# Optimization experiments

Measured on AMD Instinct MI355X. Metric: run time of the kernel, lower is better.

The kernel has to match this reference:

```python
import jax, jax.numpy as jnp
import numpy as np

N_QUBITS = 12
LAYERS = 3


def _apply(state, mats, axes):
    """Apply batched k-qubit gate. state: [B]+[2]*n complex64; mats: [B, 2^k, 2^k]; axes: state axes (1-based)."""
    k = len(axes)
    d = 2 ** k
    s = jnp.moveaxis(state, axes, tuple(range(1, k + 1)))
    shp = s.shape
    s = jnp.einsum('bij,bjk->bik', mats, s.reshape(shp[0], d, -1))
    return jnp.moveaxis(s.reshape(shp), tuple(range(1, k + 1)), axes)


def _ry(theta):
    # RY(theta) = [[cos(t/2), -sin(t/2)], [sin(t/2), cos(t/2)]], batched over B
    c = jnp.cos(theta / 2).astype(jnp.complex64)
    s = jnp.sin(theta / 2).astype(jnp.complex64)
    return jnp.stack([jnp.stack([c, -s], -1), jnp.stack([s, c], -1)], -2)


def _crx(theta):
    # CRX: identity on control=0 subspace, RX(theta) on control=1 subspace (basis order |ct>)
    c = jnp.cos(theta / 2).astype(jnp.complex64)
    s = (-1j) * jnp.sin(theta / 2).astype(jnp.complex64)
    o = jnp.ones_like(c)
    z = jnp.zeros_like(c)
    rows = [[o, z, z, z], [z, o, z, z], [z, z, c, s], [z, z, s, c]]
    return jnp.stack([jnp.stack(r, -1) for r in rows], -2)


def _circuit(state_re, state_im, params):
    B = params.shape[0]
    n = N_QUBITS
    state = (state_re + 1j * state_im).astype(jnp.complex64).reshape((B,) + (2,) * n)
    p = params.reshape(B, LAYERS, 4, n)  # param idx order: RY block, CRX block, RY block, CRX block
    for l in range(LAYERS):
        th = p[:, l]
        for w in range(n):
            state = _apply(state, _ry(th[:, 0, w]), (w + 1,))
        for i, w in enumerate(reversed(range(n))):
            state = _apply(state, _crx(th[:, 1, i]), (w + 1, ((w + 1) % n) + 1))
        for w in range(n):
            state = _apply(state, _ry(th[:, 2, w]), (w + 1,))
        for i, w in enumerate([n - 1] + list(range(n - 1))):
            state = _apply(state, _crx(th[:, 3, i]), (w + 1, ((w - 1) % n) + 1))
    state = state.reshape(B, -1)
    return jnp.stack([state.real, state.imag], -1)  # [B, 2^n, 2]


def setup_inputs() -> dict:
    key = jax.random.key(0)
    k1, k2, k3 = jax.random.split(key, 3)
    B = 128
    dim = 2 ** N_QUBITS
    return {
        'state_re': jax.random.normal(k1, (B, dim), jnp.float32),
        'state_im': jax.random.normal(k2, (B, dim), jnp.float32),
        'params': jax.random.normal(k3, (B, LAYERS * 4 * N_QUBITS), jnp.float32),
    }


def reference(state_re, state_im, params):
    return _circuit(state_re, state_im, params)
```

## Files before the change

### kernel.cpp

```cpp
#include <hip/hip_runtime.h>
#include <math.h>

#define DIM  4096
#define BLK  512
#define NPAR 144

typedef float v2f __attribute__((ext_vector_type(2)));

struct Ph { int reg[3]; int wav[3]; };
struct TMap { unsigned pk[9]; unsigned short so[8]; unsigned short rn[8]; };

constexpr int REGS[12][3] = {
  {11,0,1},{1,2,3},{3,4,5},{5,6,7},{7,8,9},{9,10,11},
  {11,0,1},{9,10,11},{7,8,9},{5,6,7},{3,4,5},{1,2,3}};

constexpr Ph phaseAt(int i) {
  Ph p = {};
  if (i == 0 || i == 37) {
    p.reg[0]=0; p.reg[1]=1; p.reg[2]=2;
    p.wav[0]=9; p.wav[1]=10; p.wav[2]=11;
    return p;
  }
  int e = (i - 1) % 12;
  for (int j = 0; j < 3; ++j) p.reg[j] = REGS[e][j];
  bool A = (e <= 2) || (e >= 10);
  p.wav[0] = A ? 6 : 2; p.wav[1] = A ? 7 : 3; p.wav[2] = A ? 8 : 4;
  return p;
}
constexpr bool inArr(const int* a, int n, int b) {
  for (int i = 0; i < n; ++i) if (a[i] == b) return true;
  return false;
}
constexpr bool isLoc(int t) {
  if (t == 0 || t == 36) return false;
  Ph a = phaseAt(t), b = phaseAt(t + 1);
  return a.wav[0]==b.wav[0] && a.wav[1]==b.wav[1] && a.wav[2]==b.wav[2];
}
constexpr int bufIdx(int t) {
  int k = 0;
  for (int u = 0; u <= t; ++u) if (!isLoc(u)) ++k;
  return (k + 1) & 1;
}

struct BuildOut { TMap m; bool ok; };

constexpr BuildOut buildT(Ph o, Ph n, bool local) {
  BuildOut R = {};
  R.ok = true;
  bool lo[12] = {}, ln[12] = {};
  for (int b = 0; b < 12; ++b) {
    lo[b] = !inArr(o.reg,3,b) && !inArr(o.wav,3,b);
    ln[b] = !inArr(n.reg,3,b) && !inArr(n.wav,3,b);
  }
  int col[12] = {};
  bool uo[12] = {}, un[12] = {}, inBank[12] = {}, pairA[12] = {};
  int row = 0;
  for (int b = 0; b < 12 && row < 4; ++b)
    if (lo[b] && ln[b]) { col[b] |= 1 << row; uo[b]=un[b]=true; inBank[b]=true; ++row; }
  while (row < 4) {
    int a = -1, c = -1;
    for (int b = 0; b < 12; ++b) if (lo[b] && !uo[b]) { a = b; break; }
    for (int b = 0; b < 12; ++b) if (ln[b] && !un[b]) { c = b; break; }
    if (a < 0 || c < 0 || a == c) { R.ok = false; return R; }
    col[a] |= 1 << row; col[c] |= 1 << row;
    uo[a]=true; un[c]=true; inBank[a]=true; inBank[c]=true; pairA[a]=true;
    ++row;
  }
  bool idset[12] = {};
  int nid = 0;
  for (int b = 0; b < 12; ++b) { idset[b] = !inBank[b] || pairA[b]; if (idset[b]) ++nid; }
  if (nid != 8) { R.ok = false; return R; }
  if (local) {
    for (int i = 0; i < 3; ++i) {
      if (!idset[o.wav[i]]) { R.ok = false; return R; }
      col[o.wav[i]] |= 1 << (9 + i);
      idset[o.wav[i]] = false;
    }
    int rr = 4;
    for (int b = 0; b < 12; ++b) if (idset[b]) { col[b] |= 1 << rr; ++rr; }
    if (rr != 9) { R.ok = false; return R; }
  } else {
    int rr = 4;
    for (int b = 0; b < 12; ++b) if (idset[b]) { col[b] |= 1 << rr; ++rr; }
    if (rr != 12) { R.ok = false; return R; }
  }
  {
    int pv[12] = {}, pb[12] = {};
    int nr = 0;
    for (int b = 0; b < 12; ++b) {
      int v = col[b];
      for (int k = 0; k < nr; ++k) if (v & pb[k]) v ^= pv[k];
      if (v) { pb[nr] = v & (-v); pv[nr] = v; ++nr; }
    }
    if (nr != 12) { R.ok = false; return R; }
  }
  int Lo[6] = {}, Ln[6] = {};
  int i0 = 0, i1 = 0;
  for (int b = 0; b < 12; ++b) { if (lo[b]) Lo[i0++] = b; if (ln[b]) Ln[i1++] = b; }
  for (int i = 0; i < 9; ++i) {
    unsigned po = (i < 6) ? (unsigned)col[Lo[i]] : (unsigned)col[o.wav[i-6]];
    unsigned pn = (i < 6) ? (unsigned)col[Ln[i]] : (unsigned)col[n.wav[i-6]];
    R.m.pk[i] = po | (pn << 16);
  }
  for (int r = 0; r < 8; ++r) {
    int s = 0, t2 = 0;
    for (int j = 0; j < 3; ++j)
      if ((r >> j) & 1) { s ^= col[o.reg[j]]; t2 ^= col[n.reg[j]]; }
    R.m.so[r] = (unsigned short)(s * 8);
    R.m.rn[r] = (unsigned short)(t2 * 8);
  }
  return R;
}

struct AllT { TMap t[37]; bool loc[37]; int buf[37]; bool ok; };
constexpr AllT buildAll() {
  AllT A = {};
  A.ok = true;
  for (int t = 0; t < 37; ++t) {
    BuildOut b = buildT(phaseAt(t), phaseAt(t + 1), isLoc(t));
    A.t[t] = b.m;
    A.ok = A.ok && b.ok;
    A.loc[t] = isLoc(t);
    A.buf[t] = bufIdx(t);
  }
  return A;
}
constexpr AllT AT = buildAll();
static_assert(AT.ok, "slot-map construction failed");

template<int J>
__device__ __forceinline__ void ry8(v2f (&z)[8], v2f a) {
  const float c = a.x, s = a.y;
  #pragma unroll
  for (int p = 0; p < 4; ++p) {
    const int r0 = ((p & ~((1 << J) - 1)) << 1) | (p & ((1 << J) - 1));
    const int r1 = r0 | (1 << J);
    v2f u = z[r0], v = z[r1];
    z[r0] = c * u - s * v;
    z[r1] = s * u + c * v;
  }
}
template<int JC, int JT>
__device__ __forceinline__ void crx8(v2f (&z)[8], v2f a) {
  const float c = a.x, s = a.y;
  constexpr int MC = 1 << JC, MT = 1 << JT;
  constexpr int mlo = MC < MT ? MC : MT;
  constexpr int mhi = MC < MT ? MT : MC;
  #pragma unroll
  for (int p = 0; p < 2; ++p) {
    int q = ((p & ~(mlo - 1)) << 1) | (p & (mlo - 1));
    q = ((q & ~(mhi - 1)) << 1) | (q & (mhi - 1));
    const int r0 = q | MC, r1 = r0 | MT;
    v2f u = z[r0], v = z[r1];
    v2f n0, n1;
    n0.x = c * u.x + s * v.y;
    n0.y = c * u.y - s * v.x;
    n1.x = c * v.x + s * u.y;
    n1.y = c * v.y - s * u.x;
    z[r0] = n0; z[r1] = n1;
  }
}

template<int E>
__device__ __forceinline__ void gates(v2f (&z)[8], const v2f* ang, int base) {
  auto A = [&](int k) { return ang[base + k]; };
  if constexpr (E == 0)      { ry8<0>(z,A(0));  ry8<1>(z,A(11)); ry8<2>(z,A(10));
                               crx8<1,0>(z,A(12)); crx8<2,1>(z,A(13)); }
  else if constexpr (E == 1) { ry8<1>(z,A(9));  ry8<2>(z,A(8));
                               crx8<1,0>(z,A(14)); crx8<2,1>(z,A(15)); }
  else if constexpr (E == 2) { ry8<1>(z,A(7));  ry8<2>(z,A(6));
                               crx8<1,0>(z,A(16)); crx8<2,1>(z,A(17)); }
  else if constexpr (E == 3) { ry8<1>(z,A(5));  ry8<2>(z,A(4));
                               crx8<1,0>(z,A(18)); crx8<2,1>(z,A(19)); }
  else if constexpr (E == 4) { ry8<1>(z,A(3));  ry8<2>(z,A(2));
                               crx8<1,0>(z,A(20)); crx8<2,1>(z,A(21)); }
  else if constexpr (E == 5) { ry8<1>(z,A(1));
                               crx8<1,0>(z,A(22)); crx8<2,1>(z,A(23)); }
  else if constexpr (E == 6) { ry8<0>(z,A(24)); ry8<1>(z,A(35)); ry8<2>(z,A(34));
                               crx8<1,2>(z,A(36)); crx8<0,1>(z,A(37)); }
  else if constexpr (E == 7) { ry8<0>(z,A(26)); ry8<1>(z,A(25));
                               crx8<1,2>(z,A(38)); crx8<0,1>(z,A(39)); }
  else if constexpr (E == 8) { ry8<0>(z,A(28)); ry8<1>(z,A(27));
                               crx8<1,2>(z,A(40)); crx8<0,1>(z,A(41)); }
  else if constexpr (E == 9) { ry8<0>(z,A(30)); ry8<1>(z,A(29));
                               crx8<1,2>(z,A(42)); crx8<0,1>(z,A(43)); }
  else if constexpr (E == 10){ ry8<0>(z,A(32)); ry8<1>(z,A(31));
                               crx8<1,2>(z,A(44)); crx8<0,1>(z,A(45)); }
  else                       { ry8<1>(z,A(33));
                               crx8<1,2>(z,A(46)); crx8<0,1>(z,A(47)); }
}

template<int T>
__device__ __forceinline__ void restage(v2f (&z)[8], int tid, char* Lb, char* C0, char* C1) {
  constexpr bool LOC = AT.loc[T];
  char* buf = LOC ? Lb : (AT.buf[T] ? C1 : C0);
  unsigned acc = 0;
  #pragma unroll
  for (int i = 0; i < 9; ++i)
    acc ^= (unsigned)(-((tid >> i) & 1)) & AT.t[T].pk[i];
  const unsigned bo = (acc & 0xfffu) << 3;
  const unsigned bn = ((acc >> 16) & 0xfffu) << 3;
  #pragma unroll
  for (int r = 0; r < 8; ++r)
    *(v2f*)(buf + (bo ^ AT.t[T].so[r])) = z[r];
  if (LOC) { asm volatile("s_waitcnt lgkmcnt(0)" ::: "memory"); }
  else     { __syncthreads(); }
  #pragma unroll
  for (int r = 0; r < 8; ++r)
    z[r] = *(const v2f*)(buf + (bn ^ AT.t[T].rn[r]));
}

template<int L>
__device__ __forceinline__ void layer(v2f (&z)[8], int tid, const v2f* ang,
                                      char* Lb, char* C0, char* C1) {
  const int base = 48 * L;
  gates<0>(z, ang, base);  restage<12*L + 1>(z, tid, Lb, C0, C1);
  gates<1>(z, ang, base);  restage<12*L + 2>(z, tid, Lb, C0, C1);
  gates<2>(z, ang, base);  restage<12*L + 3>(z, tid, Lb, C0, C1);
  gates<3>(z, ang, base);  restage<12*L + 4>(z, tid, Lb, C0, C1);
  gates<4>(z, ang, base);  restage<12*L + 5>(z, tid, Lb, C0, C1);
  gates<5>(z, ang, base);  restage<12*L + 6>(z, tid, Lb, C0, C1);
  gates<6>(z, ang, base);  restage<12*L + 7>(z, tid, Lb, C0, C1);
  gates<7>(z, ang, base);  restage<12*L + 8>(z, tid, Lb, C0, C1);
  gates<8>(z, ang, base);  restage<12*L + 9>(z, tid, Lb, C0, C1);
  gates<9>(z, ang, base);  restage<12*L + 10>(z, tid, Lb, C0, C1);
  gates<10>(z, ang, base); restage<12*L + 11>(z, tid, Lb, C0, C1);
  gates<11>(z, ang, base);
  if constexpr (L < 2) restage<12*L + 12>(z, tid, Lb, C0, C1);
}

__global__ __launch_bounds__(BLK) void ansatz_kernel(
    const float* __restrict__ sre, const float* __restrict__ sim,
    const float* __restrict__ params, float* __restrict__ out) {

  __shared__ v2f C0s[DIM], C1s[DIM], Ls[DIM];
  __shared__ v2f ang[NPAR];

  const int b = blockIdx.x, tid = threadIdx.x;
  char* C0 = (char*)C0s;
  char* C1 = (char*)C1s;
  char* Lb = (char*)Ls;

  if (tid < NPAR) {
    float s, c;
    sincosf(0.5f * params[b * NPAR + tid], &s, &c);
    v2f a; a.x = c; a.y = s;
    ang[tid] = a;
  }

  v2f z[8];
  {
    const float4* pr = (const float4*)(sre + b * DIM + (tid << 3));
    const float4* pi = (const float4*)(sim + b * DIM + (tid << 3));
    float4 fr[2], fi[2];
    fr[0] = pr[0]; fr[1] = pr[1];
    fi[0] = pi[0]; fi[1] = pi[1];
    unsigned acc = 0;
    #pragma unroll
    for (int i = 0; i < 9; ++i)
      acc ^= (unsigned)(-((tid >> i) & 1)) & AT.t[0].pk[i];
    const unsigned bo = (acc & 0xfffu) << 3;
    const unsigned bn = ((acc >> 16) & 0xfffu) << 3;
    #pragma unroll
    for (int r = 0; r < 8; ++r) {
      const float* f0 = (const float*)&fr[r >> 2];
      const float* f1 = (const float*)&fi[r >> 2];
      v2f v; v.x = f0[r & 3]; v.y = f1[r & 3];
      *(v2f*)(C0 + (bo ^ AT.t[0].so[r])) = v;
    }
    __syncthreads();
    #pragma unroll
    for (int r = 0; r < 8; ++r)
      z[r] = *(const v2f*)(C0 + (bn ^ AT.t[0].rn[r]));
  }

  layer<0>(z, tid, ang, Lb, C0, C1);
  layer<1>(z, tid, ang, Lb, C0, C1);
  layer<2>(z, tid, ang, Lb, C0, C1);

  {
    unsigned acc = 0;
    #pragma unroll
    for (int i = 0; i < 9; ++i)
      acc ^= (unsigned)(-((tid >> i) & 1)) & AT.t[36].pk[i];
    const unsigned bo = (acc & 0xfffu) << 3;
    const unsigned bn = ((acc >> 16) & 0xfffu) << 3;
    char* buf = AT.buf[36] ? C1 : C0;
    #pragma unroll
    for (int r = 0; r < 8; ++r)
      *(v2f*)(buf + (bo ^ AT.t[36].so[r])) = z[r];
    __syncthreads();
    v2f* o2 = (v2f*)out + (size_t)b * DIM + (tid << 3);
    #pragma unroll
    for (int r = 0; r < 8; r += 2) {
      v2f v0 = *(const v2f*)(buf + (bn ^ AT.t[36].rn[r]));
      v2f v1 = *(const v2f*)(buf + (bn ^ AT.t[36].rn[r + 1]));
      float4 w; w.x = v0.x; w.y = v0.y; w.z = v1.x; w.w = v1.y;
      *(float4*)(o2 + r) = w;
    }
  }
}

extern "C" void kernel_launch(void* const* d_in, const int* in_sizes, int n_in,
                              void* d_out, int out_size, void* d_ws, size_t ws_size,
                              hipStream_t stream) {
  const float* sre    = (const float*)d_in[0];
  const float* sim    = (const float*)d_in[1];
  const float* params = (const float*)d_in[2];
  float* out          = (float*)d_out;

  const int B = in_sizes[0] / DIM;
  ansatz_kernel<<<B, BLK, 0, stream>>>(sre, sim, params, out);
}
```

Before: 84.11 us.

## Rebuild LDS slot maps so restaging uses 128-bit shared-memory accesses

The compile-time slot-map builder now pins the one qubit bit shared by consecutive register phases to the lowest LDS address bit. Each thread's amplitude pairs then sit next to each other, so every restage issues four ds_write_b128 and four ds_read_b128 per thread instead of eight 64-bit accesses. The entry and exit transposes now reuse the generic restage routine. The explicit lgkmcnt wait in local restages is replaced by a compiler-only memory barrier, relying on in-order LDS execution within a wavefront. The trade-off is possibly different bank-conflict patterns for 128-bit accesses, plus a correctness risk from dropping the explicit wait.

```diff
diff --git a/kernel.cpp b/kernel.cpp
--- a/kernel.cpp
+++ b/kernel.cpp
@@ -31,6 +31,10 @@
   for (int i = 0; i < n; ++i) if (a[i] == b) return true;
   return false;
 }
+constexpr int idxOf3(const int* a, int v) {
+  for (int j = 0; j < 3; ++j) if (a[j] == v) return j;
+  return -1;
+}
 constexpr bool isLoc(int t) {
   if (t == 0 || t == 36) return false;
   Ph a = phaseAt(t), b = phaseAt(t + 1);
@@ -41,47 +45,53 @@
   for (int u = 0; u <= t; ++u) if (!isLoc(u)) ++k;
   return (k + 1) & 1;
 }
-
-struct BuildOut { TMap m; bool ok; };
+constexpr int sharedBit(Ph o, Ph n) {
+  for (int j = 0; j < 3; ++j) if (inArr(n.reg, 3, o.reg[j])) return o.reg[j];
+  return -1;
+}
+
+struct BuildOut { TMap m; int js, jn; bool ok; };
 
 constexpr BuildOut buildT(Ph o, Ph n, bool local) {
   BuildOut R = {};
   R.ok = true;
+  int s = sharedBit(o, n);
+  if (s < 0) { R.ok = false; return R; }
+  R.js = idxOf3(o.reg, s);
+  R.jn = idxOf3(n.reg, s);
+  if (R.js < 0 || R.jn < 0) { R.ok = false; return R; }
   bool lo[12] = {}, ln[12] = {};
   for (int b = 0; b < 12; ++b) {
     lo[b] = !inArr(o.reg,3,b) && !inArr(o.wav,3,b);
     ln[b] = !inArr(n.reg,3,b) && !inArr(n.wav,3,b);
   }
   int col[12] = {};
-  bool uo[12] = {}, un[12] = {}, inBank[12] = {}, pairA[12] = {};
-  int row = 0;
+  bool uo[12] = {}, un[12] = {}, consumed[12] = {};
+  col[s] = 1; consumed[s] = true;
+  int row = 1;
   for (int b = 0; b < 12 && row < 4; ++b)
-    if (lo[b] && ln[b]) { col[b] |= 1 << row; uo[b]=un[b]=true; inBank[b]=true; ++row; }
+    if (lo[b] && ln[b]) { col[b] = 1 << row; uo[b]=un[b]=true; consumed[b]=true; ++row; }
   while (row < 4) {
     int a = -1, c = -1;
-    for (int b = 0; b < 12; ++b) if (lo[b] && !uo[b]) { a = b; break; }
-    for (int b = 0; b < 12; ++b) if (ln[b] && !un[b]) { c = b; break; }
-    if (a < 0 || c < 0 || a == c) { R.ok = false; return R; }
+    for (int b = 0; b < 12; ++b) if (lo[b] && !uo[b] && !consumed[b]) { a = b; break; }
+    for (int b = 0; b < 12; ++b) if (ln[b] && !un[b] && !consumed[b] && b != a) { c = b; break; }
+    if (a < 0 || c < 0) { R.ok = false; return R; }
     col[a] |= 1 << row; col[c] |= 1 << row;
-    uo[a]=true; un[c]=true; inBank[a]=true; inBank[c]=true; pairA[a]=true;
+    uo[a]=true; un[c]=true; consumed[c]=true;
     ++row;
   }
-  bool idset[12] = {};
-  int nid = 0;
-  for (int b = 0; b < 12; ++b) { idset[b] = !inBank[b] || pairA[b]; if (idset[b]) ++nid; }
-  if (nid != 8) { R.ok = false; return R; }
   if (local) {
     for (int i = 0; i < 3; ++i) {
-      if (!idset[o.wav[i]]) { R.ok = false; return R; }
+      if (consumed[o.wav[i]]) { R.ok = false; return R; }
       col[o.wav[i]] |= 1 << (9 + i);
-      idset[o.wav[i]] = false;
+      consumed[o.wav[i]] = true;
     }
     int rr = 4;
-    for (int b = 0; b < 12; ++b) if (idset[b]) { col[b] |= 1 << rr; ++rr; }
+    for (int b = 0; b < 12; ++b) if (!consumed[b]) { col[b] |= 1 << rr; ++rr; }
     if (rr != 9) { R.ok = false; return R; }
   } else {
     int rr = 4;
-    for (int b = 0; b < 12; ++b) if (idset[b]) { col[b] |= 1 << rr; ++rr; }
+    for (int b = 0; b < 12; ++b) if (!consumed[b]) { col[b] |= 1 << rr; ++rr; }
     if (rr != 12) { R.ok = false; return R; }
   }
   {
@@ -97,22 +107,23 @@
   int Lo[6] = {}, Ln[6] = {};
   int i0 = 0, i1 = 0;
   for (int b = 0; b < 12; ++b) { if (lo[b]) Lo[i0++] = b; if (ln[b]) Ln[i1++] = b; }
+  if (i0 != 6 || i1 != 6) { R.ok = false; return R; }
   for (int i = 0; i < 9; ++i) {
     unsigned po = (i < 6) ? (unsigned)col[Lo[i]] : (unsigned)col[o.wav[i-6]];
     unsigned pn = (i < 6) ? (unsigned)col[Ln[i]] : (unsigned)col[n.wav[i-6]];
     R.m.pk[i] = po | (pn << 16);
   }
   for (int r = 0; r < 8; ++r) {
-    int s = 0, t2 = 0;
+    int a = 0, c = 0;
     for (int j = 0; j < 3; ++j)
-      if ((r >> j) & 1) { s ^= col[o.reg[j]]; t2 ^= col[n.reg[j]]; }
-    R.m.so[r] = (unsigned short)(s * 8);
-    R.m.rn[r] = (unsigned short)(t2 * 8);
+      if ((r >> j) & 1) { a ^= col[o.reg[j]]; c ^= col[n.reg[j]]; }
+    R.m.so[r] = (unsigned short)(a * 8);
+    R.m.rn[r] = (unsigned short)(c * 8);
   }
   return R;
 }
 
-struct AllT { TMap t[37]; bool loc[37]; int buf[37]; bool ok; };
+struct AllT { TMap t[37]; bool loc[37]; int buf[37]; int js[37]; int jn[37]; bool ok; };
 constexpr AllT buildAll() {
   AllT A = {};
   A.ok = true;
@@ -122,6 +133,8 @@
     A.ok = A.ok && b.ok;
     A.loc[t] = isLoc(t);
     A.buf[t] = bufIdx(t);
+    A.js[t] = b.js;
+    A.jn[t] = b.jn;
   }
   return A;
 }
@@ -193,6 +206,7 @@
 template<int T>
 __device__ __forceinline__ void restage(v2f (&z)[8], int tid, char* Lb, char* C0, char* C1) {
   constexpr bool LOC = AT.loc[T];
+  constexpr int JS = AT.js[T], JN = AT.jn[T];
   char* buf = LOC ? Lb : (AT.buf[T] ? C1 : C0);
   unsigned acc = 0;
   #pragma unroll
@@ -201,13 +215,27 @@
   const unsigned bo = (acc & 0xfffu) << 3;
   const unsigned bn = ((acc >> 16) & 0xfffu) << 3;
   #pragma unroll
-  for (int r = 0; r < 8; ++r)
-    *(v2f*)(buf + (bo ^ AT.t[T].so[r])) = z[r];
-  if (LOC) { asm volatile("s_waitcnt lgkmcnt(0)" ::: "memory"); }
-  else     { __syncthreads(); }
-  #pragma unroll
-  for (int r = 0; r < 8; ++r)
-    z[r] = *(const v2f*)(buf + (bn ^ AT.t[T].rn[r]));
+  for (int r = 0; r < 8; ++r) {
+    if (r & (1 << JS)) continue;
+    v2f z0 = z[r], z1 = z[r | (1 << JS)];
+    float4 w; w.x = z0.x; w.y = z0.y; w.z = z1.x; w.w = z1.y;
+    *(float4*)(buf + (bo ^ AT.t[T].so[r])) = w;
+  }
+  if (LOC) {
+    asm volatile("" ::: "memory");
+  } else {
+    __syncthreads();
+  }
+  #pragma unroll
+  for (int r = 0; r < 8; ++r) {
+    if (r & (1 << JN)) continue;
+    float4 w = *(const float4*)(buf + (bn ^ AT.t[T].rn[r]));
+    v2f z0, z1;
+    z0.x = w.x; z0.y = w.y;
+    z1.x = w.z; z1.y = w.w;
+    z[r] = z0;
+    z[r | (1 << JN)] = z1;
+  }
 }
 
 template<int L>
@@ -233,7 +261,7 @@
     const float* __restrict__ sre, const float* __restrict__ sim,
     const float* __restrict__ params, float* __restrict__ out) {
 
-  __shared__ v2f C0s[DIM], C1s[DIM], Ls[DIM];
+  __shared__ alignas(16) v2f C0s[DIM], C1s[DIM], Ls[DIM];
   __shared__ v2f ang[NPAR];
 
   const int b = blockIdx.x, tid = threadIdx.x;
@@ -252,52 +280,31 @@
   {
     const float4* pr = (const float4*)(sre + b * DIM + (tid << 3));
     const float4* pi = (const float4*)(sim + b * DIM + (tid << 3));
-    float4 fr[2], fi[2];
-    fr[0] = pr[0]; fr[1] = pr[1];
-    fi[0] = pi[0]; fi[1] = pi[1];
-    unsigned acc = 0;
-    #pragma unroll
-    for (int i = 0; i < 9; ++i)
-      acc ^= (unsigned)(-((tid >> i) & 1)) & AT.t[0].pk[i];
-    const unsigned bo = (acc & 0xfffu) << 3;
-    const unsigned bn = ((acc >> 16) & 0xfffu) << 3;
-    #pragma unroll
-    for (int r = 0; r < 8; ++r) {
-      const float* f0 = (const float*)&fr[r >> 2];
-      const float* f1 = (const float*)&fi[r >> 2];
-      v2f v; v.x = f0[r & 3]; v.y = f1[r & 3];
-      *(v2f*)(C0 + (bo ^ AT.t[0].so[r])) = v;
-    }
-    __syncthreads();
-    #pragma unroll
-    for (int r = 0; r < 8; ++r)
-      z[r] = *(const v2f*)(C0 + (bn ^ AT.t[0].rn[r]));
+    float4 fr0 = pr[0], fr1 = pr[1];
+    float4 fi0 = pi[0], fi1 = pi[1];
+    z[0].x = fr0.x; z[0].y = fi0.x;
+    z[1].x = fr0.y; z[1].y = fi0.y;
+    z[2].x = fr0.z; z[2].y = fi0.z;
+    z[3].x = fr0.w; z[3].y = fi0.w;
+    z[4].x = fr1.x; z[4].y = fi1.x;
+    z[5].x = fr1.y; z[5].y = fi1.y;
+    z[6].x = fr1.z; z[6].y = fi1.z;
+    z[7].x = fr1.w; z[7].y = fi1.w;
+    restage<0>(z, tid, Lb, C0, C1);
   }
 
   layer<0>(z, tid, ang, Lb, C0, C1);
   layer<1>(z, tid, ang, Lb, C0, C1);
   layer<2>(z, tid, ang, Lb, C0, C1);
 
-  {
-    unsigned acc = 0;
-    #pragma unroll
-    for (int i = 0; i < 9; ++i)
-      acc ^= (unsigned)(-((tid >> i) & 1)) & AT.t[36].pk[i];
-    const unsigned bo = (acc & 0xfffu) << 3;
-    const unsigned bn = ((acc >> 16) & 0xfffu) << 3;
-    char* buf = AT.buf[36] ? C1 : C0;
-    #pragma unroll
-    for (int r = 0; r < 8; ++r)
-      *(v2f*)(buf + (bo ^ AT.t[36].so[r])) = z[r];
-    __syncthreads();
-    v2f* o2 = (v2f*)out + (size_t)b * DIM + (tid << 3);
-    #pragma unroll
-    for (int r = 0; r < 8; r += 2) {
-      v2f v0 = *(const v2f*)(buf + (bn ^ AT.t[36].rn[r]));
-      v2f v1 = *(const v2f*)(buf + (bn ^ AT.t[36].rn[r + 1]));
-      float4 w; w.x = v0.x; w.y = v0.y; w.z = v1.x; w.w = v1.y;
-      *(float4*)(o2 + r) = w;
-    }
+  restage<36>(z, tid, Lb, C0, C1);
+  v2f* o2 = (v2f*)out + (size_t)b * DIM + (tid << 3);
+  #pragma unroll
+  for (int r = 0; r < 8; r += 2) {
+    float4 w;
+    w.x = z[r].x;     w.y = z[r].y;
+    w.z = z[r + 1].x; w.w = z[r + 1].y;
+    *(float4*)(o2 + r) = w;
   }
 }
 
```

After: 80.74 us. 1.04x faster.
